# Optimization experiments

Hardware: AMD Instinct MI355X
Metric: run time of the kernel (lower is better)

Reference implementation:

```python
import jax, jax.numpy as jnp
import numpy as np

NH, D, MULT, NLAYER = 8, 512, 32, 3
N_INT = D * MULT // NH  # 2048 sparse-code dim per head
EPS = 1e-5
THETA = 2.0 ** 16
NUM_CLASSES = 2


def _ln(x):
    # LayerNorm over last dim, no affine (elementwise_affine=False), biased var
    m = jnp.mean(x, axis=-1, keepdims=True)
    v = jnp.mean((x - m) ** 2, axis=-1, keepdims=True)
    return (x - m) * jax.lax.rsqrt(v + EPS)


def _rotate_half(x):
    x1, x2 = jnp.split(x, 2, axis=-1)
    return jnp.concatenate((-x2, x1), axis=-1)


def _attn(Qs, V):
    # Qs: [B,nh,T,N] ReLU-sparse codes (Q == K), V: [B,1,T,D] raw hidden
    T = Qs.shape[2]
    half = 1.0 / (THETA ** (jnp.arange(0, N_INT, 2, dtype=jnp.float32) / N_INT))
    freqs = jnp.concatenate((half, half))                      # [N]
    ph = jnp.arange(T, dtype=jnp.float32)[:, None] * freqs[None, :]  # [T,N]
    QR = Qs * jnp.cos(ph) + _rotate_half(Qs) * jnp.sin(ph)
    scores = jnp.einsum('bhtn,bhsn->bhts', QR, QR)             # no softmax, no scaling
    mask = jnp.tril(jnp.ones((T, T), dtype=scores.dtype), k=-1)  # strictly causal
    scores = scores * mask
    return jnp.einsum('bhts,bsd->bhtd', scores, V[:, 0])       # [B,nh,T,D]


def setup_inputs():
    key = jax.random.key(0)
    ks = jax.random.split(key, 8)
    B, T, NA, F = 2, 1024, 93, 4
    in_dim, out_dim = NA * F, NA * NUM_CLASSES
    s = 0.02
    return dict(
        x=jax.random.normal(ks[0], (B, T, NA, F), dtype=jnp.float32),
        Wi=jax.random.normal(ks[1], (in_dim, D), dtype=jnp.float32) * s,
        bi=jnp.zeros((D,), jnp.float32),
        enc=jax.random.uniform(ks[2], (NH, D, N_INT), jnp.float32, -s, s),
        enc_v=jax.random.uniform(ks[3], (NH, D, N_INT), jnp.float32, -s, s),
        dec=jax.random.uniform(ks[4], (NH * N_INT, D), jnp.float32, -s, s),
        Wo=jax.random.normal(ks[5], (D, out_dim), dtype=jnp.float32) * s,
        bo=jnp.zeros((out_dim,), jnp.float32),
    )


def reference(x, Wi, bi, enc, enc_v, dec, Wo, bo):
    B, T, NA, F = x.shape
    h = _ln((x.reshape(B, T, NA * F) @ Wi + bi)[:, None])      # [B,1,T,D]
    for _ in range(NLAYER):
        h_res = h
        h_sp = jax.nn.relu(jnp.einsum('bxtd,hdn->bhtn', h, enc))      # [B,nh,T,N]
        yKV = _ln(_attn(h_sp, h))                                     # [B,nh,T,D]
        y_sp = jax.nn.relu(jnp.einsum('bhtd,hdn->bhtn', yKV, enc_v))  # [B,nh,T,N]
        xy = h_sp * y_sp                                              # gating
        # transpose(1,2).reshape(B,1,T,nh*N): head-major flatten of codes
        xy_flat = xy.transpose(0, 2, 1, 3).reshape(B, 1, T, NH * N_INT)
        h = _ln(h_res + _ln(xy_flat @ dec))                           # [B,1,T,D]
    out = h[:, 0] @ Wo + bo                                           # [B,T,NA*C]
    return out.reshape(B, T, NA, NUM_CLASSES)
```

## Files before the change

kernel.cpp:

```cpp
#include <hip/hip_runtime.h>

typedef __bf16 bf16;
typedef __attribute__((ext_vector_type(8))) __bf16 bf16x8;
typedef __attribute__((ext_vector_type(4))) float f32x4;

#define T_SEQ 1024
#define D_MODEL 512
#define N_INT 2048
#define NHEADS 8
#define IN_DIM 372
#define IN_PAD 384
#define OUT_DIM 186
#define OUT_PAD 256

__device__ inline void gld16(const bf16* g, bf16* l) {
  __builtin_amdgcn_global_load_lds((const __attribute__((address_space(1))) void*)g,
                                   (__attribute__((address_space(3))) void*)l, 16, 0, 0);
}

__device__ inline void block_sum2(float& a, float& b, float* red) {
#pragma unroll
  for (int o = 32; o > 0; o >>= 1) {
    a += __shfl_down(a, o, 64);
    b += __shfl_down(b, o, 64);
  }
  __syncthreads();
  if ((threadIdx.x & 63) == 0) {
    int w = threadIdx.x >> 6;
    red[2 * w] = a;
    red[2 * w + 1] = b;
  }
  __syncthreads();
  a = red[0] + red[2] + red[4] + red[6];
  b = red[1] + red[3] + red[5] + red[7];
}

__global__ __launch_bounds__(256) void transpose_cvt(const float* __restrict__ in,
                                                     bf16* __restrict__ out,
                                                     int rows, int cols) {
  __shared__ float tile[32][33];
  size_t zoff = (size_t)blockIdx.z * rows * cols;
  in += zoff;
  out += zoff;
  int c0 = blockIdx.x * 32, r0 = blockIdx.y * 32;
#pragma unroll
  for (int i = threadIdx.y; i < 32; i += 8)
    tile[i][threadIdx.x] = in[(size_t)(r0 + i) * cols + c0 + threadIdx.x];
  __syncthreads();
#pragma unroll
  for (int i = threadIdx.y; i < 32; i += 8)
    out[(size_t)(c0 + i) * rows + r0 + threadIdx.x] = (bf16)tile[threadIdx.x][i];
}

__global__ __launch_bounds__(256) void pad_trans(const float* __restrict__ in,
                                                 bf16* __restrict__ out,
                                                 int R, int C, int outLd) {
  __shared__ float tile[32][33];
  int c0 = blockIdx.x * 32, r0 = blockIdx.y * 32;
#pragma unroll
  for (int i = threadIdx.y; i < 32; i += 8) {
    int r = r0 + i, c = c0 + threadIdx.x;
    tile[i][threadIdx.x] = (r < R && c < C) ? in[(size_t)r * C + c] : 0.f;
  }
  __syncthreads();
#pragma unroll
  for (int i = threadIdx.y; i < 32; i += 8)
    out[(size_t)(c0 + i) * outLd + r0 + threadIdx.x] = (bf16)tile[threadIdx.x][i];
}

__global__ __launch_bounds__(256) void cvt_pad_x(const float* __restrict__ x,
                                                 bf16* __restrict__ xbf) {
  size_t r = blockIdx.x;
  for (int c = threadIdx.x; c < IN_PAD; c += 256)
    xbf[r * IN_PAD + c] = (c < IN_DIM) ? (bf16)x[r * IN_DIM + c] : (bf16)0.f;
}

__global__ __launch_bounds__(256) void rope_tables(float* __restrict__ ct, float* __restrict__ st) {
  int t = blockIdx.x;
  for (int i = threadIdx.x; i < 1024; i += 256) {
    float ph = (float)t * exp2f(-16.0f * (float)i * (1.0f / 1024.0f));
    ct[(size_t)t * 1024 + i] = cosf(ph);
    st[(size_t)t * 1024 + i] = sinf(ph);
  }
}

__global__ __launch_bounds__(256) void rope_apply(const bf16* __restrict__ hsp,
                                                  const float* __restrict__ ct,
                                                  const float* __restrict__ st,
                                                  bf16* __restrict__ qr) {
  size_t row = (size_t)blockIdx.x * 2 + (threadIdx.x >> 7);
  int i = threadIdx.x & 127;
  int t = (int)(row & (T_SEQ - 1));
  const bf16* src = hsp + row * N_INT;
  bf16* dst = qr + row * N_INT;
  int n1 = i * 8;
  bf16x8 x1 = *(const bf16x8*)(src + n1);
  bf16x8 x2 = *(const bf16x8*)(src + n1 + 1024);
  const float* cp = ct + (size_t)t * 1024 + n1;
  const float* sp = st + (size_t)t * 1024 + n1;
  bf16x8 o1, o2;
#pragma unroll
  for (int j = 0; j < 8; ++j) {
    float c = cp[j], s = sp[j];
    float a = (float)x1[j], b = (float)x2[j];
    o1[j] = (bf16)(a * c - b * s);
    o2[j] = (bf16)(b * c + a * s);
  }
  *(bf16x8*)(dst + n1) = o1;
  *(bf16x8*)(dst + n1 + 1024) = o2;
}

__global__ __launch_bounds__(256) void psum16(const bf16* __restrict__ part,
                                              float* __restrict__ zb) {
  size_t r = blockIdx.x;
  for (int cc = threadIdx.x; cc < 512; cc += 256) {
    float s = 0.f;
#pragma unroll
    for (int k = 0; k < 16; ++k)
      s += (float)part[((size_t)k << 19) + r * 512 + cc];
    zb[r * 512 + cc] = s;
  }
}

__global__ __launch_bounds__(256) void ln0(const float* __restrict__ zin,
                                           float* __restrict__ h, bf16* __restrict__ hbf,
                                           bf16* __restrict__ hT) {
  __shared__ float red[8];
  size_t r = blockIdx.x;
  int tid = threadIdx.x;
  float v0 = zin[r * 512 + tid], v1 = zin[r * 512 + tid + 256];
  float s = v0 + v1, s2 = v0 * v0 + v1 * v1;
  block_sum2(s, s2, red);
  float mean = s * (1.f / 512.f);
  float var = s2 * (1.f / 512.f) - mean * mean;
  float rs = rsqrtf(var + 1e-5f);
  float o0 = (v0 - mean) * rs, o1 = (v1 - mean) * rs;
  h[r * 512 + tid] = o0;
  h[r * 512 + tid + 256] = o1;
  hbf[r * 512 + tid] = (bf16)o0;
  hbf[r * 512 + tid + 256] = (bf16)o1;
  int b = (int)(r >> 10), t = (int)(r & (T_SEQ - 1));
  hT[((size_t)b * 512 + tid) * T_SEQ + t] = (bf16)o0;
  hT[((size_t)b * 512 + tid + 256) * T_SEQ + t] = (bf16)o1;
}

__global__ __launch_bounds__(256) void ln_rows(bf16* __restrict__ io) {
  __shared__ float red[8];
  size_t r = blockIdx.x;
  int tid = threadIdx.x;
  float v0 = (float)io[r * 512 + tid], v1 = (float)io[r * 512 + tid + 256];
  float s = v0 + v1, s2 = v0 * v0 + v1 * v1;
  block_sum2(s, s2, red);
  float mean = s * (1.f / 512.f);
  float var = s2 * (1.f / 512.f) - mean * mean;
  float rs = rsqrtf(var + 1e-5f);
  io[r * 512 + tid] = (bf16)((v0 - mean) * rs);
  io[r * 512 + tid + 256] = (bf16)((v1 - mean) * rs);
}

__global__ __launch_bounds__(256) void ln_double(const float* __restrict__ zin,
                                                 float* __restrict__ h, bf16* __restrict__ hbf,
                                                 bf16* __restrict__ hT) {
  __shared__ float red[8];
  size_t r = blockIdx.x;
  int tid = threadIdx.x;
  float z0 = zin[r * 512 + tid], z1 = zin[r * 512 + tid + 256];
  float s = z0 + z1, s2 = z0 * z0 + z1 * z1;
  block_sum2(s, s2, red);
  float m1 = s * (1.f / 512.f);
  float v1_ = s2 * (1.f / 512.f) - m1 * m1;
  float rs1 = rsqrtf(v1_ + 1e-5f);
  float a0 = (z0 - m1) * rs1 + h[r * 512 + tid];
  float a1 = (z1 - m1) * rs1 + h[r * 512 + tid + 256];
  s = a0 + a1;
  s2 = a0 * a0 + a1 * a1;
  block_sum2(s, s2, red);
  float m2 = s * (1.f / 512.f);
  float v2_ = s2 * (1.f / 512.f) - m2 * m2;
  float rs2 = rsqrtf(v2_ + 1e-5f);
  float o0 = (a0 - m2) * rs2, o1 = (a1 - m2) * rs2;
  h[r * 512 + tid] = o0;
  h[r * 512 + tid + 256] = o1;
  hbf[r * 512 + tid] = (bf16)o0;
  hbf[r * 512 + tid + 256] = (bf16)o1;
  int b = (int)(r >> 10), t = (int)(r & (T_SEQ - 1));
  hT[((size_t)b * 512 + tid) * T_SEQ + t] = (bf16)o0;
  hT[((size_t)b * 512 + tid + 256) * T_SEQ + t] = (bf16)o1;
}

template <int MODE, int GX, int TILE>
__device__ __forceinline__ void gemm_body(const bf16* __restrict__ Abase,
                                          const bf16* __restrict__ Bbase,
                                          const bf16* __restrict__ aux,
                                          const float* __restrict__ fbias,
                                          float* __restrict__ fout,
                                          bf16* __restrict__ bout) {
  const int id = blockIdx.x;
  int bz = 0, r_, chunk = 0;
  if constexpr (MODE >= 5) {
    r_ = id;
  } else if constexpr (MODE == 4) {
    r_ = id & 31;
    chunk = id >> 5;
  } else {
    bz = id & 7;
    r_ = id >> 3;
  }
  int bi, bj;
  if constexpr (MODE == 1) {
    int l = r_;
    float f = sqrtf(8.0f * (float)l + 1.0f);
    bi = (int)((f - 1.0f) * 0.5f);
    while ((bi + 1) * (bi + 2) / 2 <= l) ++bi;
    while (bi * (bi + 1) / 2 > l) --bi;
    bj = l - bi * (bi + 1) / 2;
  } else {
    bi = r_ % GX;
    bj = r_ / GX;
  }

  const bf16* A;
  const bf16* Bt;
  int lda, ldb, kend;
  if constexpr (MODE == 0) {
    A = Abase; lda = 512;
    Bt = Bbase + (size_t)bz * N_INT * 512; ldb = 512;
    kend = 512;
  } else if constexpr (MODE == 1) {
    A = Abase + (size_t)bz * T_SEQ * N_INT; lda = N_INT;
    Bt = A; ldb = N_INT;
    kend = N_INT;
  } else if constexpr (MODE == 2) {
    A = Abase + (size_t)bz * T_SEQ * T_SEQ; lda = T_SEQ;
    Bt = Bbase; ldb = T_SEQ;
    kend = (bi + 1) * TILE;
  } else if constexpr (MODE == 3) {
    A = Abase + (size_t)bz * T_SEQ * 512; lda = 512;
    Bt = Bbase + (size_t)bz * N_INT * 512; ldb = 512;
    kend = 512;
  } else if constexpr (MODE == 4) {
    A = Abase + (size_t)chunk * 1024; lda = 16384;
    Bt = Bbase + (size_t)chunk * 1024; ldb = 16384;
    kend = 1024;
  } else if constexpr (MODE == 5) {
    A = Abase; lda = IN_PAD;
    Bt = Bbase; ldb = IN_PAD;
    kend = IN_PAD;
  } else {
    A = Abase; lda = 512;
    Bt = Bbase; ldb = 512;
    kend = 512;
  }

  const int tid = threadIdx.x;
  constexpr int PASSES = TILE / 32;
  const int trow = tid >> 3, tq = tid & 7;
  const int sq = tq ^ (trow & 7);
  const bf16* ags = A + (size_t)(bi * TILE + trow) * lda + sq * 8;
  const bf16* bgs = Bt + (size_t)(bj * TILE + trow) * ldb + sq * 8;

  __shared__ __align__(16) bf16 As[2][TILE * 64];
  __shared__ __align__(16) bf16 Bs[2][TILE * 64];
  const int so = tid * 8;

  const int lane = tid & 63, wid = tid >> 6;
  const int wr = wid >> 1, wc = wid & 1;
  const int fr = lane & 15, fg = lane >> 4;
  const int axor = fr & 7;
  constexpr int MR = TILE / 32;

  f32x4 acc[MR][MR] = {};

  auto stage = [&](int buf, int kk) {
#pragma unroll
    for (int p = 0; p < PASSES; ++p) {
      gld16(ags + (size_t)(p * 32) * lda + kk, &As[buf][p * 2048 + so]);
      gld16(bgs + (size_t)(p * 32) * ldb + kk, &Bs[buf][p * 2048 + so]);
    }
  };

  const int nt = kend >> 6;
  stage(0, 0);

  for (int t = 0; t < nt; ++t) {
    const int cur = t & 1;
    if (t + 1 < nt) {
      stage(cur ^ 1, (t + 1) << 6);
      if constexpr (TILE == 128)
        asm volatile("s_waitcnt vmcnt(8)" ::: "memory");
      else
        asm volatile("s_waitcnt vmcnt(4)" ::: "memory");
    } else {
      asm volatile("s_waitcnt vmcnt(0)" ::: "memory");
    }
    __builtin_amdgcn_sched_barrier(0);
    __builtin_amdgcn_s_barrier();
    __builtin_amdgcn_sched_barrier(0);

    __builtin_amdgcn_s_setprio(1);
#pragma unroll
    for (int s = 0; s < 2; ++s) {
      bf16x8 af[MR], bfv[MR];
#pragma unroll
      for (int m = 0; m < MR; ++m)
        af[m] = *(const bf16x8*)(&As[cur][(wr * (TILE / 2) + m * 16 + fr) * 64 + (((s * 4 + fg) ^ axor) * 8)]);
#pragma unroll
      for (int n = 0; n < MR; ++n)
        bfv[n] = *(const bf16x8*)(&Bs[cur][(wc * (TILE / 2) + n * 16 + fr) * 64 + (((s * 4 + fg) ^ axor) * 8)]);
#pragma unroll
      for (int m = 0; m < MR; ++m)
#pragma unroll
        for (int n = 0; n < MR; ++n)
          acc[m][n] = __builtin_amdgcn_mfma_f32_16x16x32_bf16(af[m], bfv[n], acc[m][n], 0, 0, 0);
    }
    __builtin_amdgcn_s_setprio(0);

    asm volatile("s_waitcnt lgkmcnt(0)" ::: "memory");
    __builtin_amdgcn_sched_barrier(0);
    __builtin_amdgcn_s_barrier();
    __builtin_amdgcn_sched_barrier(0);
  }

#pragma unroll
  for (int m = 0; m < MR; ++m) {
#pragma unroll
    for (int n = 0; n < MR; ++n) {
#pragma unroll
      for (int j = 0; j < 4; ++j) {
        int r = bi * TILE + wr * (TILE / 2) + m * 16 + fg * 4 + j;
        int c = bj * TILE + wc * (TILE / 2) + n * 16 + fr;
        float v = acc[m][n][j];
        if constexpr (MODE == 0) {
          v = fmaxf(v, 0.f);
          bout[((size_t)bz * T_SEQ + r) * N_INT + c] = (bf16)v;
        } else if constexpr (MODE == 1) {
          bout[(size_t)bz * T_SEQ * T_SEQ + (size_t)r * T_SEQ + c] = (bf16)(c < r ? v : 0.f);
        } else if constexpr (MODE == 2) {
          bout[((size_t)bz * T_SEQ + r) * 512 + c] = (bf16)v;
        } else if constexpr (MODE == 3) {
          v = fmaxf(v, 0.f);
          float g = (float)aux[((size_t)bz * T_SEQ + r) * N_INT + c];
          bout[(size_t)r * 16384 + (size_t)bz * N_INT + c] = (bf16)(v * g);
        } else if constexpr (MODE == 4) {
          bout[((size_t)chunk << 19) + (size_t)r * 512 + c] = (bf16)v;
        } else if constexpr (MODE == 5) {
          fout[(size_t)r * 512 + c] = v + fbias[c];
        } else {
          if (c < OUT_DIM) fout[(size_t)r * OUT_DIM + c] = v + fbias[c];
        }
      }
    }
  }
}

__global__ __launch_bounds__(256, 2) void g_hsp(const bf16* A, const bf16* B, bf16* o) {
  gemm_body<0, 8, 128>(A, B, nullptr, nullptr, nullptr, o);
}
__global__ __launch_bounds__(256, 4) void g_scores(const bf16* A, bf16* o) {
  gemm_body<1, 0, 64>(A, nullptr, nullptr, nullptr, nullptr, o);
}
__global__ __launch_bounds__(256, 4) void g_pv(const bf16* A, const bf16* B, bf16* o) {
  gemm_body<2, 16, 64>(A, B, nullptr, nullptr, nullptr, o);
}
__global__ __launch_bounds__(256, 2) void g_gate(const bf16* A, const bf16* B, const bf16* aux, bf16* o) {
  gemm_body<3, 8, 128>(A, B, aux, nullptr, nullptr, o);
}
__global__ __launch_bounds__(256, 2) void g_dec(const bf16* A, const bf16* B, bf16* o) {
  gemm_body<4, 8, 128>(A, B, nullptr, nullptr, nullptr, o);
}
__global__ __launch_bounds__(256, 2) void g_in(const bf16* A, const bf16* B, const float* bias, float* o) {
  gemm_body<5, 16, 128>(A, B, nullptr, bias, o, nullptr);
}
__global__ __launch_bounds__(256, 2) void g_out(const bf16* A, const bf16* B, const float* bias, float* o) {
  gemm_body<6, 16, 128>(A, B, nullptr, bias, o, nullptr);
}

extern "C" void kernel_launch(void* const* d_in, const int* in_sizes, int n_in,
                              void* d_out, int out_size, void* d_ws, size_t ws_size,
                              hipStream_t stream) {
  const float* x = (const float*)d_in[0];
  const float* Wi = (const float*)d_in[1];
  const float* bi = (const float*)d_in[2];
  const float* enc = (const float*)d_in[3];
  const float* encv = (const float*)d_in[4];
  const float* dec = (const float*)d_in[5];
  const float* Wo = (const float*)d_in[6];
  const float* bo = (const float*)d_in[7];
  float* out = (float*)d_out;

  const size_t NEED = 163840000;
  if (ws_size < NEED) return;

  char* w = (char*)d_ws;
  auto alloc = [&](size_t bytes) {
    char* p = w;
    w += (bytes + 255) & ~(size_t)255;
    return p;
  };
  bf16* encT = (bf16*)alloc((size_t)NHEADS * N_INT * 512 * 2);
  bf16* encvT = (bf16*)alloc((size_t)NHEADS * N_INT * 512 * 2);
  bf16* decT = (bf16*)alloc((size_t)512 * 16384 * 2);
  float* cost = (float*)alloc((size_t)T_SEQ * 1024 * 4);
  float* sint = (float*)alloc((size_t)T_SEQ * 1024 * 4);
  float* h = (float*)alloc((size_t)2048 * 512 * 4);
  bf16* hbf = (bf16*)alloc((size_t)2048 * 512 * 2);
  bf16* hT = (bf16*)alloc((size_t)2048 * 512 * 2);
  bf16* hsp = (bf16*)alloc((size_t)NHEADS * T_SEQ * N_INT * 2);
  bf16* qr = (bf16*)alloc((size_t)NHEADS * T_SEQ * N_INT * 2);
  bf16* S = (bf16*)alloc((size_t)NHEADS * T_SEQ * T_SEQ * 2);
  bf16* ykv = (bf16*)alloc((size_t)NHEADS * T_SEQ * 512 * 2);
  float* zbuf = (float*)alloc((size_t)2048 * 512 * 4);
  bf16* WoT = (bf16*)alloc((size_t)OUT_PAD * 512 * 2);
  bf16* xbf = S;
  bf16* WiT = S + 1048576;

  transpose_cvt<<<dim3(64, 16, 8), dim3(32, 8), 0, stream>>>(enc, encT, 512, N_INT);
  transpose_cvt<<<dim3(64, 16, 8), dim3(32, 8), 0, stream>>>(encv, encvT, 512, N_INT);
  transpose_cvt<<<dim3(16, 512, 1), dim3(32, 8), 0, stream>>>(dec, decT, 16384, 512);
  pad_trans<<<dim3(16, 12), dim3(32, 8), 0, stream>>>(Wi, WiT, IN_DIM, 512, IN_PAD);
  pad_trans<<<dim3(8, 16), dim3(32, 8), 0, stream>>>(Wo, WoT, 512, OUT_DIM, 512);
  cvt_pad_x<<<2048, 256, 0, stream>>>(x, xbf);
  rope_tables<<<1024, 256, 0, stream>>>(cost, sint);
  g_in<<<64, 256, 0, stream>>>(xbf, WiT, bi, zbuf);
  ln0<<<2048, 256, 0, stream>>>(zbuf, h, hbf, hT);

  for (int L = 0; L < 3; ++L) {
    for (int b = 0; b < 2; ++b) {
      const bf16* hbf_b = hbf + (size_t)b * T_SEQ * 512;
      const bf16* hT_b = hT + (size_t)b * 512 * T_SEQ;
      float* zbuf_b = zbuf + (size_t)b * T_SEQ * 512;
      g_hsp<<<1024, 256, 0, stream>>>(hbf_b, encT, hsp);
      rope_apply<<<4096, 256, 0, stream>>>(hsp, cost, sint, qr);
      g_scores<<<1088, 256, 0, stream>>>(qr, S);
      g_pv<<<1024, 256, 0, stream>>>(S, hT_b, ykv);
      ln_rows<<<8192, 256, 0, stream>>>(ykv);
      g_gate<<<1024, 256, 0, stream>>>(ykv, encvT, hsp, qr);
      g_dec<<<512, 256, 0, stream>>>(qr, decT, S);
      psum16<<<1024, 256, 0, stream>>>(S, zbuf_b);
    }
    ln_double<<<2048, 256, 0, stream>>>(zbuf, h, hbf, hT);
  }
  g_out<<<32, 256, 0, stream>>>(hbf, WoT, bo, out);
}
```

Before: 1.025 ms.

## Fuse RoPE into sparse-code GEMM epilogue and triple-buffer scores/PV GEMMs

Adds a dedicated h_sp GEMM kernel whose tile pairs column n with column n+1024, so the ReLU output and its rotary embedding can both be written from the epilogue. This removes the separate rope_apply pass, which re-read h_sp and the cos/sin tables. It also gives the gemm template a pipeline-depth parameter and switches the scores and PV GEMMs to three LDS buffers with a two-stage-ahead prefetch, lowering their occupancy hint from 4 to 3. The epilogue stores are scattered bf16 writes with per-element table loads, which may be poorly coalesced.

New measurement: 1.055 ms. 1.03x slower.

```diff
diff --git a/kernel.cpp b/kernel.cpp
--- a/kernel.cpp
+++ b/kernel.cpp
@@ -82,32 +82,6 @@
     ct[(size_t)t * 1024 + i] = cosf(ph);
     st[(size_t)t * 1024 + i] = sinf(ph);
   }
-}
-
-__global__ __launch_bounds__(256) void rope_apply(const bf16* __restrict__ hsp,
-                                                  const float* __restrict__ ct,
-                                                  const float* __restrict__ st,
-                                                  bf16* __restrict__ qr) {
-  size_t row = (size_t)blockIdx.x * 2 + (threadIdx.x >> 7);
-  int i = threadIdx.x & 127;
-  int t = (int)(row & (T_SEQ - 1));
-  const bf16* src = hsp + row * N_INT;
-  bf16* dst = qr + row * N_INT;
-  int n1 = i * 8;
-  bf16x8 x1 = *(const bf16x8*)(src + n1);
-  bf16x8 x2 = *(const bf16x8*)(src + n1 + 1024);
-  const float* cp = ct + (size_t)t * 1024 + n1;
-  const float* sp = st + (size_t)t * 1024 + n1;
-  bf16x8 o1, o2;
-#pragma unroll
-  for (int j = 0; j < 8; ++j) {
-    float c = cp[j], s = sp[j];
-    float a = (float)x1[j], b = (float)x2[j];
-    o1[j] = (bf16)(a * c - b * s);
-    o2[j] = (bf16)(b * c + a * s);
-  }
-  *(bf16x8*)(dst + n1) = o1;
-  *(bf16x8*)(dst + n1 + 1024) = o2;
 }
 
 __global__ __launch_bounds__(256) void psum16(const bf16* __restrict__ part,
@@ -188,7 +162,114 @@
   hT[((size_t)b * 512 + tid + 256) * T_SEQ + t] = (bf16)o1;
 }
 
-template <int MODE, int GX, int TILE>
+__global__ __launch_bounds__(256, 2) void g_hspr(const bf16* __restrict__ hbf_b,
+                                                 const bf16* __restrict__ encT,
+                                                 const float* __restrict__ ct,
+                                                 const float* __restrict__ st,
+                                                 bf16* __restrict__ hsp,
+                                                 bf16* __restrict__ qr) {
+  const int id = blockIdx.x;
+  const int bz = id & 7;
+  const int r_ = id >> 3;
+  const int bi = r_ & 7;
+  const int bj = r_ >> 3;
+
+  const bf16* B0 = encT + (size_t)bz * N_INT * 512 + (size_t)(bj * 64) * 512;
+  const bf16* B1 = B0 + (size_t)1024 * 512;
+
+  const int tid = threadIdx.x;
+  const int trow = tid >> 3, tq = tid & 7;
+  const int sq = tq ^ (trow & 7);
+  const bf16* ags = hbf_b + (size_t)(bi * 128 + trow) * 512 + sq * 8;
+  const bf16* bgs0 = B0 + (size_t)trow * 512 + sq * 8;
+  const bf16* bgs1 = B1 + (size_t)trow * 512 + sq * 8;
+
+  __shared__ __align__(16) bf16 As[2][128 * 64];
+  __shared__ __align__(16) bf16 Bs[2][2 * 64 * 64];
+  const int so = tid * 8;
+
+  const int lane = tid & 63, wid = tid >> 6;
+  const int wr = wid >> 1, wc = wid & 1;
+  const int fr = lane & 15, fg = lane >> 4;
+  const int axor = fr & 7;
+
+  f32x4 acc[4][2][2] = {};
+
+  auto stage = [&](int buf, int kk) {
+#pragma unroll
+    for (int p = 0; p < 4; ++p)
+      gld16(ags + (size_t)(p * 32) * 512 + kk, &As[buf][p * 2048 + so]);
+    gld16(bgs0 + kk, &Bs[buf][0 * 2048 + so]);
+    gld16(bgs0 + (size_t)32 * 512 + kk, &Bs[buf][1 * 2048 + so]);
+    gld16(bgs1 + kk, &Bs[buf][2 * 2048 + so]);
+    gld16(bgs1 + (size_t)32 * 512 + kk, &Bs[buf][3 * 2048 + so]);
+  };
+
+  stage(0, 0);
+  for (int t = 0; t < 8; ++t) {
+    const int cur = t & 1;
+    if (t + 1 < 8) {
+      stage(cur ^ 1, (t + 1) << 6);
+      asm volatile("s_waitcnt vmcnt(8)" ::: "memory");
+    } else {
+      asm volatile("s_waitcnt vmcnt(0)" ::: "memory");
+    }
+    __builtin_amdgcn_sched_barrier(0);
+    __builtin_amdgcn_s_barrier();
+    __builtin_amdgcn_sched_barrier(0);
+
+    __builtin_amdgcn_s_setprio(1);
+#pragma unroll
+    for (int s = 0; s < 2; ++s) {
+      bf16x8 af[4], bfv[2][2];
+#pragma unroll
+      for (int m = 0; m < 4; ++m)
+        af[m] = *(const bf16x8*)(&As[cur][(wr * 64 + m * 16 + fr) * 64 + (((s * 4 + fg) ^ axor) * 8)]);
+#pragma unroll
+      for (int pp = 0; pp < 2; ++pp)
+#pragma unroll
+        for (int n = 0; n < 2; ++n)
+          bfv[pp][n] = *(const bf16x8*)(&Bs[cur][pp * 4096 + (wc * 32 + n * 16 + fr) * 64 + (((s * 4 + fg) ^ axor) * 8)]);
+#pragma unroll
+      for (int m = 0; m < 4; ++m)
+#pragma unroll
+        for (int n = 0; n < 2; ++n)
+#pragma unroll
+          for (int pp = 0; pp < 2; ++pp)
+            acc[m][n][pp] = __builtin_amdgcn_mfma_f32_16x16x32_bf16(af[m], bfv[pp][n], acc[m][n][pp], 0, 0, 0);
+    }
+    __builtin_amdgcn_s_setprio(0);
+
+    asm volatile("s_waitcnt lgkmcnt(0)" ::: "memory");
+    __builtin_amdgcn_sched_barrier(0);
+    __builtin_amdgcn_s_barrier();
+    __builtin_amdgcn_sched_barrier(0);
+  }
+
+  const size_t hb = (size_t)bz * T_SEQ;
+#pragma unroll
+  for (int m = 0; m < 4; ++m) {
+#pragma unroll
+    for (int n = 0; n < 2; ++n) {
+      int c = bj * 64 + wc * 32 + n * 16 + fr;
+#pragma unroll
+      for (int j = 0; j < 4; ++j) {
+        int r = bi * 128 + wr * 64 + m * 16 + fg * 4 + j;
+        float v0 = fmaxf(acc[m][n][0][j], 0.f);
+        float v1 = fmaxf(acc[m][n][1][j], 0.f);
+        float co = ct[(size_t)r * 1024 + c];
+        float si = st[(size_t)r * 1024 + c];
+        size_t base = (hb + r) * N_INT + c;
+        hsp[base] = (bf16)v0;
+        hsp[base + 1024] = (bf16)v1;
+        qr[base] = (bf16)(v0 * co - v1 * si);
+        qr[base + 1024] = (bf16)(v1 * co + v0 * si);
+      }
+    }
+  }
+}
+
+template <int MODE, int GX, int TILE, int DEPTH>
 __device__ __forceinline__ void gemm_body(const bf16* __restrict__ Abase,
                                           const bf16* __restrict__ Bbase,
                                           const bf16* __restrict__ aux,
@@ -222,11 +303,7 @@
   const bf16* A;
   const bf16* Bt;
   int lda, ldb, kend;
-  if constexpr (MODE == 0) {
-    A = Abase; lda = 512;
-    Bt = Bbase + (size_t)bz * N_INT * 512; ldb = 512;
-    kend = 512;
-  } else if constexpr (MODE == 1) {
+  if constexpr (MODE == 1) {
     A = Abase + (size_t)bz * T_SEQ * N_INT; lda = N_INT;
     Bt = A; ldb = N_INT;
     kend = N_INT;
@@ -254,13 +331,14 @@
 
   const int tid = threadIdx.x;
   constexpr int PASSES = TILE / 32;
+  constexpr int NBUF = DEPTH + 1;
   const int trow = tid >> 3, tq = tid & 7;
   const int sq = tq ^ (trow & 7);
   const bf16* ags = A + (size_t)(bi * TILE + trow) * lda + sq * 8;
   const bf16* bgs = Bt + (size_t)(bj * TILE + trow) * ldb + sq * 8;
 
-  __shared__ __align__(16) bf16 As[2][TILE * 64];
-  __shared__ __align__(16) bf16 Bs[2][TILE * 64];
+  __shared__ __align__(16) bf16 As[NBUF][TILE * 64];
+  __shared__ __align__(16) bf16 Bs[NBUF][TILE * 64];
   const int so = tid * 8;
 
   const int lane = tid & 63, wid = tid >> 6;
@@ -281,17 +359,31 @@
 
   const int nt = kend >> 6;
   stage(0, 0);
+  if constexpr (DEPTH == 2) {
+    if (nt > 1) stage(1, 64);
+  }
 
   for (int t = 0; t < nt; ++t) {
-    const int cur = t & 1;
-    if (t + 1 < nt) {
-      stage(cur ^ 1, (t + 1) << 6);
-      if constexpr (TILE == 128)
-        asm volatile("s_waitcnt vmcnt(8)" ::: "memory");
-      else
-        asm volatile("s_waitcnt vmcnt(4)" ::: "memory");
+    const int cur = (DEPTH == 2) ? (t % 3) : (t & 1);
+    if constexpr (DEPTH == 2) {
+      if (t + 2 < nt) {
+        stage((t + 2) % 3, (t + 2) << 6);
+        if constexpr (TILE == 64) asm volatile("s_waitcnt vmcnt(8)" ::: "memory");
+        else asm volatile("s_waitcnt vmcnt(16)" ::: "memory");
+      } else if (t + 1 < nt) {
+        if constexpr (TILE == 64) asm volatile("s_waitcnt vmcnt(4)" ::: "memory");
+        else asm volatile("s_waitcnt vmcnt(8)" ::: "memory");
+      } else {
+        asm volatile("s_waitcnt vmcnt(0)" ::: "memory");
+      }
     } else {
-      asm volatile("s_waitcnt vmcnt(0)" ::: "memory");
+      if (t + 1 < nt) {
+        stage(cur ^ 1, (t + 1) << 6);
+        if constexpr (TILE == 64) asm volatile("s_waitcnt vmcnt(4)" ::: "memory");
+        else asm volatile("s_waitcnt vmcnt(8)" ::: "memory");
+      } else {
+        asm volatile("s_waitcnt vmcnt(0)" ::: "memory");
+      }
     }
     __builtin_amdgcn_sched_barrier(0);
     __builtin_amdgcn_s_barrier();
@@ -330,10 +422,7 @@
         int r = bi * TILE + wr * (TILE / 2) + m * 16 + fg * 4 + j;
         int c = bj * TILE + wc * (TILE / 2) + n * 16 + fr;
         float v = acc[m][n][j];
-        if constexpr (MODE == 0) {
-          v = fmaxf(v, 0.f);
-          bout[((size_t)bz * T_SEQ + r) * N_INT + c] = (bf16)v;
-        } else if constexpr (MODE == 1) {
+        if constexpr (MODE == 1) {
           bout[(size_t)bz * T_SEQ * T_SEQ + (size_t)r * T_SEQ + c] = (bf16)(c < r ? v : 0.f);
         } else if constexpr (MODE == 2) {
           bout[((size_t)bz * T_SEQ + r) * 512 + c] = (bf16)v;
@@ -353,26 +442,23 @@
   }
 }
 
-__global__ __launch_bounds__(256, 2) void g_hsp(const bf16* A, const bf16* B, bf16* o) {
-  gemm_body<0, 8, 128>(A, B, nullptr, nullptr, nullptr, o);
-}
-__global__ __launch_bounds__(256, 4) void g_scores(const bf16* A, bf16* o) {
-  gemm_body<1, 0, 64>(A, nullptr, nullptr, nullptr, nullptr, o);
-}
-__global__ __launch_bounds__(256, 4) void g_pv(const bf16* A, const bf16* B, bf16* o) {
-  gemm_body<2, 16, 64>(A, B, nullptr, nullptr, nullptr, o);
+__global__ __launch_bounds__(256, 3) void g_scores(const bf16* A, bf16* o) {
+  gemm_body<1, 0, 64, 2>(A, nullptr, nullptr, nullptr, nullptr, o);
+}
+__global__ __launch_bounds__(256, 3) void g_pv(const bf16* A, const bf16* B, bf16* o) {
+  gemm_body<2, 16, 64, 2>(A, B, nullptr, nullptr, nullptr, o);
 }
 __global__ __launch_bounds__(256, 2) void g_gate(const bf16* A, const bf16* B, const bf16* aux, bf16* o) {
-  gemm_body<3, 8, 128>(A, B, aux, nullptr, nullptr, o);
+  gemm_body<3, 8, 128, 1>(A, B, aux, nullptr, nullptr, o);
 }
 __global__ __launch_bounds__(256, 2) void g_dec(const bf16* A, const bf16* B, bf16* o) {
-  gemm_body<4, 8, 128>(A, B, nullptr, nullptr, nullptr, o);
+  gemm_body<4, 8, 128, 1>(A, B, nullptr, nullptr, nullptr, o);
 }
 __global__ __launch_bounds__(256, 2) void g_in(const bf16* A, const bf16* B, const float* bias, float* o) {
-  gemm_body<5, 16, 128>(A, B, nullptr, bias, o, nullptr);
+  gemm_body<5, 16, 128, 1>(A, B, nullptr, bias, o, nullptr);
 }
 __global__ __launch_bounds__(256, 2) void g_out(const bf16* A, const bf16* B, const float* bias, float* o) {
-  gemm_body<6, 16, 128>(A, B, nullptr, bias, o, nullptr);
+  gemm_body<6, 16, 128, 1>(A, B, nullptr, bias, o, nullptr);
 }
 
 extern "C" void kernel_launch(void* const* d_in, const int* in_sizes, int n_in,
@@ -429,8 +515,7 @@
       const bf16* hbf_b = hbf + (size_t)b * T_SEQ * 512;
       const bf16* hT_b = hT + (size_t)b * 512 * T_SEQ;
       float* zbuf_b = zbuf + (size_t)b * T_SEQ * 512;
-      g_hsp<<<1024, 256, 0, stream>>>(hbf_b, encT, hsp);
-      rope_apply<<<4096, 256, 0, stream>>>(hsp, cost, sint, qr);
+      g_hspr<<<1024, 256, 0, stream>>>(hbf_b, encT, cost, sint, hsp, qr);
       g_scores<<<1088, 256, 0, stream>>>(qr, S);
       g_pv<<<1024, 256, 0, stream>>>(S, hT_b, ykv);
       ln_rows<<<8192, 256, 0, stream>>>(ykv);
```
